# Kernel optimization log

Hardware: AMD Instinct MI355X
Metric: run time of the kernel (lower is better)

Reference implementation:

```python
import jax, jax.numpy as jnp
import numpy as np

B, H, L, N = 16, 256, 4096, 64  # N = d_state//2 retained complex-conjugate modes (S4D)
EPS = 1e-5


def setup_inputs() -> dict:
    key = jax.random.key(0)
    ks = jax.random.split(key, 6)
    x = jax.random.normal(ks[0], (B, H, L), dtype=jnp.float32)
    # dt log-uniform in [1e-3, 1e-1] per channel (standard S4 init)
    log_dt = (jax.random.uniform(ks[1], (H,), dtype=jnp.float32)
              * (np.log(0.1) - np.log(0.001)) + np.log(0.001))
    # S4D-Lin init: A_n = -1/2 + i*pi*n
    A_re = -0.5 * jnp.ones((H, N), dtype=jnp.float32)
    A_im = jnp.pi * jnp.broadcast_to(jnp.arange(N, dtype=jnp.float32), (H, N))
    # bidirectional -> 2 channel groups of C
    C_re = jax.random.normal(ks[2], (2, H, N), dtype=jnp.float32)
    C_im = jax.random.normal(ks[3], (2, H, N), dtype=jnp.float32)
    D = jax.random.normal(ks[4], (H,), dtype=jnp.float32)
    ln_w = jnp.ones((H,), dtype=jnp.float32)
    ln_b = jnp.zeros((H,), dtype=jnp.float32)
    W_out = jax.random.normal(ks[5], (H, H), dtype=jnp.float32) / np.sqrt(H)
    b_out = jnp.zeros((H,), dtype=jnp.float32)
    return {"x": x, "log_dt": log_dt, "A_re": A_re, "A_im": A_im,
            "C_re": C_re, "C_im": C_im, "D": D,
            "ln_w": ln_w, "ln_b": ln_b, "W_out": W_out, "b_out": b_out}


def _s4_forward(x, log_dt, A_re, A_im, C_re, C_im, D, ln_w, ln_b, W_out, b_out):
    # LayerNorm over channel dim (x.transpose -> LN(d_model) -> transpose back)
    mu = jnp.mean(x, axis=1, keepdims=True)
    var = jnp.mean((x - mu) ** 2, axis=1, keepdims=True)
    z = (x - mu) * jax.lax.rsqrt(var + EPS) * ln_w[None, :, None] + ln_b[None, :, None]

    # --- S4D kernel via Vandermonde (ZOH-style discretization) ---
    A = A_re + 1j * A_im                         # (H, N)
    C = C_re + 1j * C_im                         # (2, H, N)
    dt = jnp.exp(log_dt)[:, None]                # (H, 1)
    dtA = dt * A                                 # (H, N)
    C_t = C * (jnp.exp(dtA) - 1.0) / A           # (2, H, N)
    t = jnp.arange(L, dtype=jnp.float32)
    V = jnp.exp(dtA[:, :, None] * t)             # (H, N, L) Vandermonde
    K = 2.0 * jnp.real(jnp.einsum('dhn,hnl->dhl', C_t, V))  # (2, H, L)

    # bidirectional: forward kernel padded right, backward kernel flipped, padded left
    k = jnp.pad(K[0], ((0, 0), (0, L))) + jnp.pad(K[1][:, ::-1], ((0, 0), (L, 0)))

    # FFT convolution over length 2L
    Uf = jnp.fft.rfft(z, n=2 * L)                # (B, H, L+1)
    Kf = jnp.fft.rfft(k, n=2 * L)                # (H, L+1)
    y = jnp.fft.irfft(Uf * Kf[None], n=2 * L)[..., :L]

    y = y + D[None, :, None] * z                 # skip D*u
    y = jax.nn.gelu(y)                           # S4 default activation
    # transposed position-wise output linear (postact=None -> plain Linear)
    y = jnp.einsum('oh,bhl->bol', W_out, y) + b_out[None, :, None]
    return x + y                                  # residual


def reference(x, log_dt, A_re, A_im, C_re, C_im, D, ln_w, ln_b, W_out, b_out):
    return _s4_forward(x, log_dt, A_re, A_im, C_re, C_im, D, ln_w, ln_b, W_out, b_out)
```

## Files before the change

### kernel.cpp

```cpp
#include <hip/hip_runtime.h>
#include <math.h>

#define B_ 16
#define H_ 256
#define L_ 4096
#define N_ 64
#define HN (H_*N_)
#define HL (H_*L_)
#define BHL (B_*H_*L_)

#define WVT_OFS 0
#define TM_OFS  8192
#define E2T_OFS 12288
#define MATS_PER 20480

typedef short bf16x8 __attribute__((ext_vector_type(8)));
typedef float f32x4  __attribute__((ext_vector_type(4)));

__device__ __forceinline__ unsigned int pk2(float a, float b) {
    return ((__float_as_uint(a) + 0x8000u) >> 16) |
           ((__float_as_uint(b) + 0x8000u) & 0xffff0000u);
}
__device__ __forceinline__ unsigned short bfr(float a) {
    return (unsigned short)((__float_as_uint(a) + 0x8000u) >> 16);
}
__device__ __forceinline__ float ubf(unsigned short u) {
    return __uint_as_float(((unsigned int)u) << 16);
}

__global__ void __launch_bounds__(64) mats_kernel(const float* __restrict__ log_dt,
                                                  const float* __restrict__ A_re,
                                                  const float* __restrict__ A_im,
                                                  const float* __restrict__ C_re,
                                                  const float* __restrict__ C_im,
                                                  unsigned short* __restrict__ mats,
                                                  float2* __restrict__ Wc) {
    int hd = blockIdx.x;
    int h = hd >> 1, d = hd & 1;
    int m = threadIdx.x;
    __shared__ float2 pws[65 * 64];
    __shared__ float2 c2s[64];
    __shared__ float  Karr[64];

    int i = h * 64 + m;
    float dt = expf(log_dt[h]);
    float Are = A_re[i], Aim = A_im[i];
    float dr = dt * Are, di = dt * Aim;
    float er = expf(dr);
    float wr = er * cosf(di), wi = er * sinf(di);
    float em1r = wr - 1.0f, em1i = wi;
    float inv = 1.0f / (Are * Are + Aim * Aim);
    float qr = (em1r * Are + em1i * Aim) * inv;
    float qi = (em1i * Are - em1r * Aim) * inv;
    float Cr = C_re[d * HN + i], Ci = C_im[d * HN + i];
    float2 c2;
    c2.x = 2.0f * (Cr * qr - Ci * qi);
    c2.y = 2.0f * (Cr * qi + Ci * qr);
    c2s[m] = c2;
    float pr = 1.0f, pi = 0.0f;
    for (int k = 0; k < 64; ++k) {
        float2 p; p.x = pr; p.y = pi;
        pws[k * 64 + ((m + k) & 63)] = p;
        float t = pr * wr - pi * wi;
        pi = pr * wi + pi * wr;
        pr = t;
    }
    {
        float2 p; p.x = pr; p.y = pi;
        pws[64 * 64 + ((m + 64) & 63)] = p;
        Wc[hd * 64 + m] = p;
    }
    __syncthreads();
    {
        float kk = 0.f;
        for (int mm = 0; mm < 64; ++mm) {
            float2 c = c2s[mm];
            float2 pw = pws[m * 64 + ((mm + m) & 63)];
            kk += c.x * pw.x - c.y * pw.y;
        }
        Karr[m] = kk;
    }
    __syncthreads();
    unsigned short* mb = mats + (size_t)hd * MATS_PER;
    for (int i2 = 0; i2 < 32; ++i2) {
        int e0 = 2 * i2, e1 = e0 + 1;
        int k0 = d ? e0 : 63 - e0;
        int k1 = d ? e1 : 63 - e1;
        float2 p0 = pws[k0 * 64 + ((m + k0) & 63)];
        float2 p1 = pws[k1 * 64 + ((m + k1) & 63)];
        *(unsigned int*)(mb + WVT_OFS + (2 * m) * 64 + e0)     = pk2(p0.x, p1.x);
        *(unsigned int*)(mb + WVT_OFS + (2 * m + 1) * 64 + e0) = pk2(p0.y, p1.y);
    }
    for (int i2 = 0; i2 < 32; ++i2) {
        int e0 = 2 * i2, e1 = e0 + 1;
        float v0, v1;
        if (d == 0) {
            v0 = (e0 <= m) ? Karr[m - e0] : 0.f;
            v1 = (e1 <= m) ? Karr[m - e1] : 0.f;
        } else {
            v0 = (e0 > m) ? Karr[e0 - m - 1] : 0.f;
            v1 = (e1 > m) ? Karr[e1 - m - 1] : 0.f;
        }
        *(unsigned int*)(mb + TM_OFS + m * 64 + e0) = pk2(v0, v1);
    }
    {
        int kp = d ? (63 - m) : (m + 1);
        for (int mm = 0; mm < 64; ++mm) {
            float2 c = c2s[mm];
            float2 pw = pws[kp * 64 + ((mm + kp) & 63)];
            float vr = c.x * pw.x - c.y * pw.y;
            float vi = -(c.x * pw.y + c.y * pw.x);
            *(unsigned int*)(mb + E2T_OFS + m * 128 + 2 * mm) = pk2(vr, vi);
        }
    }
}

__global__ void __launch_bounds__(256) wbf_kernel(const float* __restrict__ W,
                                                  unsigned short* __restrict__ Wbf) {
    int i = (blockIdx.x * 256 + threadIdx.x) * 4;
    float4 v = *(const float4*)(W + i);
    uint2 u;
    u.x = pk2(v.x, v.y);
    u.y = pk2(v.z, v.w);
    *(uint2*)(Wbf + i) = u;
}

__global__ void __launch_bounds__(256) ln_kernel(const float* __restrict__ x,
                                                 const float* __restrict__ lnw,
                                                 const float* __restrict__ lnb,
                                                 unsigned short* __restrict__ zb) {
    int b  = blockIdx.y;
    int l0 = blockIdx.x * 256;
    int t  = threadIdx.x;
    int hq = t >> 6, lo = t & 63;
    int l  = l0 + lo * 4;
    __shared__ float4 r1[4][64];
    __shared__ float4 r2[4][64];
    __shared__ float4 muS[64];
    __shared__ float4 rsS[64];
    const float* xb = x + (size_t)b * HL;
    float4 s1 = {0.f,0.f,0.f,0.f}, s2 = {0.f,0.f,0.f,0.f};
    #pragma unroll 4
    for (int hh = 0; hh < 64; ++hh) {
        int h = hq * 64 + hh;
        float4 v = *(const float4*)(xb + (size_t)h * L_ + l);
        s1.x += v.x; s1.y += v.y; s1.z += v.z; s1.w += v.w;
        s2.x += v.x*v.x; s2.y += v.y*v.y; s2.z += v.z*v.z; s2.w += v.w*v.w;
    }
    r1[hq][lo] = s1; r2[hq][lo] = s2;
    __syncthreads();
    if (t < 64) {
        float4 S1 = r1[0][t], S2 = r2[0][t];
        #pragma unroll
        for (int q = 1; q < 4; ++q) {
            float4 a = r1[q][t], c = r2[q][t];
            S1.x += a.x; S1.y += a.y; S1.z += a.z; S1.w += a.w;
            S2.x += c.x; S2.y += c.y; S2.z += c.z; S2.w += c.w;
        }
        const float invH = 1.0f / 256.0f;
        float4 mu, rs;
        mu.x = S1.x*invH; mu.y = S1.y*invH; mu.z = S1.z*invH; mu.w = S1.w*invH;
        rs.x = rsqrtf(S2.x*invH - mu.x*mu.x + 1e-5f);
        rs.y = rsqrtf(S2.y*invH - mu.y*mu.y + 1e-5f);
        rs.z = rsqrtf(S2.z*invH - mu.z*mu.z + 1e-5f);
        rs.w = rsqrtf(S2.w*invH - mu.w*mu.w + 1e-5f);
        muS[t] = mu; rsS[t] = rs;
    }
    __syncthreads();
    float4 mu = muS[lo], rs = rsS[lo];
    #pragma unroll 4
    for (int hh = 0; hh < 64; ++hh) {
        int h = hq * 64 + hh;
        float w = lnw[h], bb = lnb[h];
        float4 v = *(const float4*)(xb + (size_t)h * L_ + l);
        float4 zz;
        zz.x = (v.x - mu.x) * rs.x * w + bb;
        zz.y = (v.y - mu.y) * rs.y * w + bb;
        zz.z = (v.z - mu.z) * rs.z * w + bb;
        zz.w = (v.w - mu.w) * rs.w * w + bb;
        uint2 u;
        u.x = pk2(zz.x, zz.y);
        u.y = pk2(zz.z, zz.w);
        *(uint2*)(zb + (size_t)b * HL + (size_t)h * L_ + l) = u;
    }
}

#define MFMA16(a,b,c) __builtin_amdgcn_mfma_f32_16x16x32_bf16((a),(b),(c),0,0,0)
#define SU_BASE 8192
#define GST_BASE 32768

__global__ void __launch_bounds__(256, 3) ssm_kernel(const unsigned short* __restrict__ zb,
                                                     const unsigned short* __restrict__ mats,
                                                     const float2* __restrict__ Wc,
                                                     const float* __restrict__ D,
                                                     unsigned short* __restrict__ gb) {
    int bh = blockIdx.x;
    int h  = bh & (H_ - 1);
    int t  = threadIdx.x;
    int w  = t >> 6, l = t & 63;
    int d  = w >> 1, p = w & 1;

    __shared__ __align__(16) char smem[40960];

    const unsigned short* mb = mats + (size_t)(h * 2 + d) * MATS_PER;

    {
        const char* zrow = (const char*)(zb + (size_t)bh * L_);
        #pragma unroll
        for (int k = 0; k < 2; ++k) {
            int row = w * 16 + k * 8 + (l >> 3);
            int chunk = (l & 7) ^ (row & 7);
            const char* src = zrow + row * 128 + chunk * 16;
            __builtin_amdgcn_global_load_lds(
                (const __attribute__((address_space(1))) unsigned int*)src,
                (__attribute__((address_space(3))) unsigned int*)(smem + w * 2048 + k * 1024),
                16, 0, 0);
        }
    }
    __syncthreads();

    bf16x8 za[4][2];
    int arow = l & 15;
    int koff = (l >> 4) * 8;
    #pragma unroll
    for (int cb = 0; cb < 4; ++cb) {
        int row = cb * 16 + arow;
        unsigned int sw = (row & 7) << 4;
        #pragma unroll
        for (int kb = 0; kb < 2; ++kb) {
            unsigned int byte = (unsigned)(row * 128 + (kb * 32 + koff) * 2) ^ sw;
            za[cb][kb] = *(bf16x8*)(smem + byte);
        }
    }

    char* sUd = smem + SU_BASE + d * 16384;
    #pragma unroll
    for (int mcb = 0; mcb < 4; ++mcb) {
        int mcblk = p * 4 + mcb;
        const unsigned short* wv = mb + WVT_OFS + (mcblk * 16 + arow) * 64 + koff;
        bf16x8 b0 = *(const bf16x8*)(wv);
        bf16x8 b1 = *(const bf16x8*)(wv + 32);
        #pragma unroll
        for (int cb = 0; cb < 4; ++cb) {
            f32x4 acc = {0.f, 0.f, 0.f, 0.f};
            acc = MFMA16(za[cb][0], b0, acc);
            acc = MFMA16(za[cb][1], b1, acc);
            int mc = mcblk * 16 + arow;
            #pragma unroll
            for (int rr = 0; rr < 4; ++rr) {
                int c = cb * 16 + (l >> 4) * 4 + rr;
                unsigned int byte = ((unsigned)(c * 256 + mc * 2)) ^ ((c & 7) << 4);
                *(unsigned short*)(sUd + byte) = bfr(acc[rr]);
            }
        }
    }
    __syncthreads();

    if (p == 0) {
        float2 w64 = Wc[(h * 2 + d) * 64 + l];
        float sr = 0.f, si = 0.f;
        if (d == 0) {
            for (int c = 0; c < 64; ++c) {
                unsigned int byte = ((unsigned)(c * 256 + l * 4)) ^ ((c & 7) << 4);
                unsigned int uu = *(unsigned int*)(sUd + byte);
                float ur = __uint_as_float(uu << 16);
                float ui = __uint_as_float(uu & 0xffff0000u);
                *(unsigned int*)(sUd + byte) = pk2(sr, si);
                float nsr = fmaf(w64.x, sr, fmaf(-w64.y, si, ur));
                float nsi = fmaf(w64.x, si, fmaf(w64.y, sr, ui));
                sr = nsr; si = nsi;
            }
        } else {
            for (int c = 63; c >= 0; --c) {
                unsigned int byte = ((unsigned)(c * 256 + l * 4)) ^ ((c & 7) << 4);
                unsigned int uu = *(unsigned int*)(sUd + byte);
                float ur = __uint_as_float(uu << 16);
                float ui = __uint_as_float(uu & 0xffff0000u);
                *(unsigned int*)(sUd + byte) = pk2(sr, si);
                float nsr = fmaf(w64.x, sr, fmaf(-w64.y, si, ur));
                float nsi = fmaf(w64.x, si, fmaf(w64.y, sr, ui));
                sr = nsr; si = nsi;
            }
        }
    }
    __syncthreads();

    f32x4 yacc[2][4];
    #pragma unroll
    for (int jb = 0; jb < 2; ++jb) {
        int jblk = p * 2 + jb;
        const unsigned short* tm = mb + TM_OFS + (jblk * 16 + arow) * 64 + koff;
        bf16x8 tb0 = *(const bf16x8*)(tm);
        bf16x8 tb1 = *(const bf16x8*)(tm + 32);
        const unsigned short* et = mb + E2T_OFS + (jblk * 16 + arow) * 128 + koff;
        bf16x8 eb0 = *(const bf16x8*)(et);
        bf16x8 eb1 = *(const bf16x8*)(et + 32);
        bf16x8 eb2 = *(const bf16x8*)(et + 64);
        bf16x8 eb3 = *(const bf16x8*)(et + 96);
        #pragma unroll
        for (int cb = 0; cb < 4; ++cb) {
            f32x4 acc = {0.f, 0.f, 0.f, 0.f};
            acc = MFMA16(za[cb][0], tb0, acc);
            acc = MFMA16(za[cb][1], tb1, acc);
            int row = cb * 16 + arow;
            unsigned int sw = (row & 7) << 4;
            bf16x8 sa0 = *(bf16x8*)(sUd + (((unsigned)(row * 256 + (0 * 32 + koff) * 2)) ^ sw));
            bf16x8 sa1 = *(bf16x8*)(sUd + (((unsigned)(row * 256 + (1 * 32 + koff) * 2)) ^ sw));
            bf16x8 sa2 = *(bf16x8*)(sUd + (((unsigned)(row * 256 + (2 * 32 + koff) * 2)) ^ sw));
            bf16x8 sa3 = *(bf16x8*)(sUd + (((unsigned)(row * 256 + (3 * 32 + koff) * 2)) ^ sw));
            acc = MFMA16(sa0, eb0, acc);
            acc = MFMA16(sa1, eb1, acc);
            acc = MFMA16(sa2, eb2, acc);
            acc = MFMA16(sa3, eb3, acc);
            yacc[jb][cb] = acc;
        }
    }
    __syncthreads();

    float* Yb = (float*)(smem + SU_BASE);
    if (d == 1) {
        #pragma unroll
        for (int jb = 0; jb < 2; ++jb) {
            int j = (p * 2 + jb) * 16 + arow;
            #pragma unroll
            for (int cb = 0; cb < 4; ++cb) {
                #pragma unroll
                for (int rr = 0; rr < 4; ++rr) {
                    int c = cb * 16 + (l >> 4) * 4 + rr;
                    Yb[c * 66 + j] = yacc[jb][cb][rr];
                }
            }
        }
    }
    __syncthreads();
    if (d == 0) {
        float dv = D[h];
        #pragma unroll
        for (int jb = 0; jb < 2; ++jb) {
            int j = (p * 2 + jb) * 16 + arow;
            #pragma unroll
            for (int cb = 0; cb < 4; ++cb) {
                #pragma unroll
                for (int rr = 0; rr < 4; ++rr) {
                    int c = cb * 16 + (l >> 4) * 4 + rr;
                    unsigned int zbyte = ((unsigned)(c * 128 + j * 2)) ^ ((c & 7) << 4);
                    float zv = ubf(*(unsigned short*)(smem + zbyte));
                    float y = yacc[jb][cb][rr] + Yb[c * 66 + j] + dv * zv;
                    float inner = 0.7978845608028654f * (y + 0.044715f * y * y * y);
                    float gv = 0.5f * y * (1.0f + tanhf(inner));
                    *(unsigned short*)(smem + GST_BASE + zbyte) = bfr(gv);
                }
            }
        }
    }
    __syncthreads();
    {
        int c2 = t >> 2, s2 = t & 3;
        unsigned int rsw = (c2 & 7) << 4;
        char* go = (char*)(gb + (size_t)bh * L_);
        uint4 a0 = *(const uint4*)(smem + GST_BASE + (((unsigned)(c2 * 128 + s2 * 32)) ^ rsw));
        uint4 a1 = *(const uint4*)(smem + GST_BASE + (((unsigned)(c2 * 128 + s2 * 32 + 16)) ^ rsw));
        *(uint4*)(go + c2 * 128 + s2 * 32)      = a0;
        *(uint4*)(go + c2 * 128 + s2 * 32 + 16) = a1;
    }
}

__global__ void __launch_bounds__(256, 4) gt_kernel(const unsigned short* __restrict__ gb,
                                                    unsigned short* __restrict__ gT) {
    int b  = blockIdx.y;
    int l0 = blockIdx.x * 64;
    int t  = threadIdx.x;
    __shared__ __align__(16) char lT[64 * 512];
    const unsigned short* gp = gb + ((size_t)b * H_ + t) * L_ + l0;
    uint4 v[8];
    #pragma unroll
    for (int j8 = 0; j8 < 8; ++j8) v[j8] = *(const uint4*)(gp + j8 * 8);
    #pragma unroll
    for (int j8 = 0; j8 < 8; ++j8) {
        #pragma unroll
        for (int e = 0; e < 8; ++e) {
            int l = j8 * 8 + e;
            unsigned short val = ((const unsigned short*)&v[j8])[e];
            *(unsigned short*)(lT + (((unsigned)(l * 512 + t * 2)) ^ ((l & 7) << 4))) = val;
        }
    }
    __syncthreads();
    int l = t >> 2, seg = t & 3;
    unsigned short* dst = gT + ((size_t)b * L_ + l0 + l) * 256 + seg * 64;
    unsigned int sw = (l & 7) << 4;
    #pragma unroll
    for (int j = 0; j < 8; ++j) {
        uint4 u = *(const uint4*)(lT + (((unsigned)(l * 512 + seg * 128 + j * 16)) ^ sw));
        *(uint4*)(dst + j * 8) = u;
    }
}

__global__ void __launch_bounds__(256, 3) outproj_kernel(
        const unsigned short* __restrict__ gT,
        const unsigned short* __restrict__ Wbf,
        const float* __restrict__ x,
        const float* __restrict__ bias,
        float* __restrict__ out) {
    int b  = blockIdx.z;
    int o0 = blockIdx.y * 128;
    int l0 = blockIdx.x * 128;
    int t  = threadIdx.x;
    int w  = t >> 6, lane = t & 63;
    int wr = w >> 1, wc = w & 1;
    int l15 = lane & 15, q = lane >> 4;

    __shared__ __align__(16) char lds[34816];
    unsigned short* At = (unsigned short*)lds;
    unsigned short* Bt = (unsigned short*)(lds + 16384);

    f32x4 acc[4][4];
    #pragma unroll
    for (int i = 0; i < 4; ++i)
        #pragma unroll
        for (int j = 0; j < 4; ++j) acc[i][j] = (f32x4){0.f, 0.f, 0.f, 0.f};

    const unsigned short* gTb = gT + ((size_t)b * L_ + l0) * 256;
    const unsigned short* Wb0 = Wbf + (size_t)o0 * 256;
    unsigned int swz = (unsigned)(l15 & 7) << 4;

    for (int kt = 0; kt < 4; ++kt) {
        int k0 = kt * 64;
        #pragma unroll
        for (int s = 0; s < 4; ++s) {
            int id = (w * 4 + s) * 64 + lane;
            int row = id >> 3, ch = id & 7;
            int chl = ch ^ (row & 7);
            uint4 va = *(const uint4*)(gTb + (size_t)row * 256 + k0 + chl * 8);
            uint4 vb = *(const uint4*)(Wb0 + (size_t)row * 256 + k0 + chl * 8);
            *(uint4*)(At + id * 8) = va;
            *(uint4*)(Bt + id * 8) = vb;
        }
        __syncthreads();
        #pragma unroll
        for (int kk = 0; kk < 2; ++kk) {
            bf16x8 af[4], bfr_[4];
            #pragma unroll
            for (int rb = 0; rb < 4; ++rb) {
                int li = wr * 64 + rb * 16 + l15;
                af[rb] = *(const bf16x8*)((char*)At + li * 128 + (((kk * 64 + q * 16)) ^ swz));
                int oi = wc * 64 + rb * 16 + l15;
                bfr_[rb] = *(const bf16x8*)((char*)Bt + oi * 128 + (((kk * 64 + q * 16)) ^ swz));
            }
            #pragma unroll
            for (int rb = 0; rb < 4; ++rb)
                #pragma unroll
                for (int cb = 0; cb < 4; ++cb)
                    acc[rb][cb] = MFMA16(af[rb], bfr_[cb], acc[rb][cb]);
        }
        __syncthreads();
    }

    float* Eb = (float*)lds;
    for (int pp = 0; pp < 2; ++pp) {
        if (wc == pp) {
            #pragma unroll
            for (int cb = 0; cb < 4; ++cb) {
                int o_loc = cb * 16 + l15;
                unsigned int esw = (unsigned)(o_loc & 7) << 4;
                #pragma unroll
                for (int rb = 0; rb < 4; ++rb) {
                    int colbase = wr * 64 + rb * 16 + q * 4;
                    #pragma unroll
                    for (int r = 0; r < 4; ++r) {
                        int col = colbase + r;
                        *(float*)((char*)Eb + o_loc * 528 + (((unsigned)(col * 4)) ^ esw)) =
                            acc[rb][cb][r];
                    }
                }
            }
        }
        __syncthreads();
        int o_loc = t >> 2, lseg = t & 3;
        int o = o0 + pp * 64 + o_loc;
        float bo = bias[o];
        unsigned int esw = (unsigned)(o_loc & 7) << 4;
        size_t off = ((size_t)b * H_ + o) * L_ + l0 + lseg * 32;
        const float* xr = x + off;
        float* orow = out + off;
        #pragma unroll
        for (int j = 0; j < 8; ++j) {
            float4 e = *(const float4*)((char*)Eb + o_loc * 528 +
                                        (((unsigned)(lseg * 128 + j * 16)) ^ esw));
            float4 xv = *(const float4*)(xr + j * 4);
            float4 ov;
            ov.x = xv.x + bo + e.x;
            ov.y = xv.y + bo + e.y;
            ov.z = xv.z + bo + e.z;
            ov.w = xv.w + bo + e.w;
            *(float4*)(orow + j * 4) = ov;
        }
        __syncthreads();
    }
}

extern "C" void kernel_launch(void* const* d_in, const int* in_sizes, int n_in,
                              void* d_out, int out_size, void* d_ws, size_t ws_size,
                              hipStream_t stream) {
    const float* x      = (const float*)d_in[0];
    const float* log_dt = (const float*)d_in[1];
    const float* A_re   = (const float*)d_in[2];
    const float* A_im   = (const float*)d_in[3];
    const float* C_re   = (const float*)d_in[4];
    const float* C_im   = (const float*)d_in[5];
    const float* D      = (const float*)d_in[6];
    const float* lnw    = (const float*)d_in[7];
    const float* lnb    = (const float*)d_in[8];
    const float* W      = (const float*)d_in[9];
    const float* bout   = (const float*)d_in[10];
    float* out = (float*)d_out;

    unsigned short* zb   = (unsigned short*)d_ws;
    unsigned short* gb   = zb + (size_t)BHL;
    unsigned short* gT   = gb + (size_t)BHL;
    unsigned short* mats = gT + (size_t)BHL;
    float2* Wc = (float2*)(mats + 512 * (size_t)MATS_PER);
    unsigned short* Wbf = (unsigned short*)(Wc + 512 * 64);

    mats_kernel<<<512, 64, 0, stream>>>(log_dt, A_re, A_im, C_re, C_im, mats, Wc);
    wbf_kernel<<<64, 256, 0, stream>>>(W, Wbf);
    ln_kernel<<<dim3(L_ / 256, B_), 256, 0, stream>>>(x, lnw, lnb, zb);
    ssm_kernel<<<B_ * H_, 256, 0, stream>>>(zb, mats, Wc, D, gb);
    gt_kernel<<<dim3(L_ / 64, B_), 256, 0, stream>>>(gb, gT);
    outproj_kernel<<<dim3(L_ / 128, H_ / 128, B_), 256, 0, stream>>>(gT, Wbf, x, bout, out);
}
```

Baseline: 208.7 us.

## Split SSM directions into separate blocks and fuse combine+GELU into transpose

Each SSM block now handles one direction (forward or backward) with 128 threads, so there are twice as many blocks, each using less shared memory, and the in-block cross-direction reduction through LDS is gone. Each block writes its partial output as bf16 to a separate buffer. The transpose kernel then reads both partials plus z, applies the D skip and a tanh-form GELU written with exp and a reciprocal, and writes the transposed result. This adds an extra BHL bf16 buffer of global traffic and rounds the partial outputs to bf16 before they are summed.

```diff
diff --git a/kernel.cpp b/kernel.cpp
--- a/kernel.cpp
+++ b/kernel.cpp
@@ -187,33 +187,34 @@
 
 #define MFMA16(a,b,c) __builtin_amdgcn_mfma_f32_16x16x32_bf16((a),(b),(c),0,0,0)
 #define SU_BASE 8192
-#define GST_BASE 32768
-
-__global__ void __launch_bounds__(256, 3) ssm_kernel(const unsigned short* __restrict__ zb,
+
+__global__ void __launch_bounds__(128, 3) ssm_kernel(const unsigned short* __restrict__ zb,
                                                      const unsigned short* __restrict__ mats,
                                                      const float2* __restrict__ Wc,
-                                                     const float* __restrict__ D,
-                                                     unsigned short* __restrict__ gb) {
-    int bh = blockIdx.x;
+                                                     unsigned short* __restrict__ yf,
+                                                     unsigned short* __restrict__ yb) {
+    int bhd = blockIdx.x;
+    int d  = bhd & 1;
+    int bh = bhd >> 1;
     int h  = bh & (H_ - 1);
     int t  = threadIdx.x;
     int w  = t >> 6, l = t & 63;
-    int d  = w >> 1, p = w & 1;
-
-    __shared__ __align__(16) char smem[40960];
+    int p  = w;
+
+    __shared__ __align__(16) char smem[24576];
 
     const unsigned short* mb = mats + (size_t)(h * 2 + d) * MATS_PER;
 
     {
         const char* zrow = (const char*)(zb + (size_t)bh * L_);
         #pragma unroll
-        for (int k = 0; k < 2; ++k) {
-            int row = w * 16 + k * 8 + (l >> 3);
+        for (int k = 0; k < 4; ++k) {
+            int row = w * 32 + k * 8 + (l >> 3);
             int chunk = (l & 7) ^ (row & 7);
             const char* src = zrow + row * 128 + chunk * 16;
             __builtin_amdgcn_global_load_lds(
                 (const __attribute__((address_space(1))) unsigned int*)src,
-                (__attribute__((address_space(3))) unsigned int*)(smem + w * 2048 + k * 1024),
+                (__attribute__((address_space(3))) unsigned int*)(smem + w * 4096 + k * 1024),
                 16, 0, 0);
         }
     }
@@ -233,7 +234,7 @@
         }
     }
 
-    char* sUd = smem + SU_BASE + d * 16384;
+    char* sUd = smem + SU_BASE;
     #pragma unroll
     for (int mcb = 0; mcb < 4; ++mcb) {
         int mcblk = p * 4 + mcb;
@@ -317,71 +318,63 @@
     }
     __syncthreads();
 
-    float* Yb = (float*)(smem + SU_BASE);
-    if (d == 1) {
-        #pragma unroll
-        for (int jb = 0; jb < 2; ++jb) {
-            int j = (p * 2 + jb) * 16 + arow;
+    #pragma unroll
+    for (int jb = 0; jb < 2; ++jb) {
+        int j = (p * 2 + jb) * 16 + arow;
+        #pragma unroll
+        for (int cb = 0; cb < 4; ++cb) {
             #pragma unroll
-            for (int cb = 0; cb < 4; ++cb) {
-                #pragma unroll
-                for (int rr = 0; rr < 4; ++rr) {
-                    int c = cb * 16 + (l >> 4) * 4 + rr;
-                    Yb[c * 66 + j] = yacc[jb][cb][rr];
-                }
+            for (int rr = 0; rr < 4; ++rr) {
+                int c = cb * 16 + (l >> 4) * 4 + rr;
+                unsigned int byte = ((unsigned)(c * 128 + j * 2)) ^ ((c & 7) << 4);
+                *(unsigned short*)(smem + byte) = bfr(yacc[jb][cb][rr]);
             }
         }
     }
     __syncthreads();
-    if (d == 0) {
-        float dv = D[h];
-        #pragma unroll
-        for (int jb = 0; jb < 2; ++jb) {
-            int j = (p * 2 + jb) * 16 + arow;
-            #pragma unroll
-            for (int cb = 0; cb < 4; ++cb) {
-                #pragma unroll
-                for (int rr = 0; rr < 4; ++rr) {
-                    int c = cb * 16 + (l >> 4) * 4 + rr;
-                    unsigned int zbyte = ((unsigned)(c * 128 + j * 2)) ^ ((c & 7) << 4);
-                    float zv = ubf(*(unsigned short*)(smem + zbyte));
-                    float y = yacc[jb][cb][rr] + Yb[c * 66 + j] + dv * zv;
-                    float inner = 0.7978845608028654f * (y + 0.044715f * y * y * y);
-                    float gv = 0.5f * y * (1.0f + tanhf(inner));
-                    *(unsigned short*)(smem + GST_BASE + zbyte) = bfr(gv);
-                }
-            }
-        }
-    }
-    __syncthreads();
     {
-        int c2 = t >> 2, s2 = t & 3;
-        unsigned int rsw = (c2 & 7) << 4;
-        char* go = (char*)(gb + (size_t)bh * L_);
-        uint4 a0 = *(const uint4*)(smem + GST_BASE + (((unsigned)(c2 * 128 + s2 * 32)) ^ rsw));
-        uint4 a1 = *(const uint4*)(smem + GST_BASE + (((unsigned)(c2 * 128 + s2 * 32 + 16)) ^ rsw));
-        *(uint4*)(go + c2 * 128 + s2 * 32)      = a0;
-        *(uint4*)(go + c2 * 128 + s2 * 32 + 16) = a1;
-    }
-}
-
-__global__ void __launch_bounds__(256, 4) gt_kernel(const unsigned short* __restrict__ gb,
+        int row = t >> 1, halfq = t & 1;
+        unsigned int rsw = (row & 7) << 4;
+        char* go = (char*)((d ? yb : yf) + (size_t)bh * L_);
+        #pragma unroll
+        for (int j = 0; j < 4; ++j) {
+            unsigned int off = (unsigned)(row * 128 + halfq * 64 + j * 16);
+            uint4 a = *(const uint4*)(smem + (off ^ rsw));
+            *(uint4*)(go + off) = a;
+        }
+    }
+}
+
+__global__ void __launch_bounds__(256, 4) gt_kernel(const unsigned short* __restrict__ yf,
+                                                    const unsigned short* __restrict__ yb,
+                                                    const unsigned short* __restrict__ zbuf,
+                                                    const float* __restrict__ D,
                                                     unsigned short* __restrict__ gT) {
     int b  = blockIdx.y;
     int l0 = blockIdx.x * 64;
     int t  = threadIdx.x;
     __shared__ __align__(16) char lT[64 * 512];
-    const unsigned short* gp = gb + ((size_t)b * H_ + t) * L_ + l0;
-    uint4 v[8];
-    #pragma unroll
-    for (int j8 = 0; j8 < 8; ++j8) v[j8] = *(const uint4*)(gp + j8 * 8);
+    size_t base = ((size_t)b * H_ + t) * L_ + l0;
+    const uint4* yfp = (const uint4*)(yf + base);
+    const uint4* ybp = (const uint4*)(yb + base);
+    const uint4* zp  = (const uint4*)(zbuf + base);
+    float dh = D[t];
     #pragma unroll
     for (int j8 = 0; j8 < 8; ++j8) {
+        uint4 a = yfp[j8];
+        uint4 c = ybp[j8];
+        uint4 z4 = zp[j8];
         #pragma unroll
         for (int e = 0; e < 8; ++e) {
             int l = j8 * 8 + e;
-            unsigned short val = ((const unsigned short*)&v[j8])[e];
-            *(unsigned short*)(lT + (((unsigned)(l * 512 + t * 2)) ^ ((l & 7) << 4))) = val;
+            float vf = ubf(((const unsigned short*)&a)[e]);
+            float vb = ubf(((const unsigned short*)&c)[e]);
+            float vz = ubf(((const unsigned short*)&z4)[e]);
+            float y = vf + vb + dh * vz;
+            float inner = 0.7978845608028654f * (y + 0.044715f * y * y * y);
+            float en = __expf(-2.0f * inner);
+            float g = y * __builtin_amdgcn_rcpf(1.0f + en);
+            *(unsigned short*)(lT + (((unsigned)(l * 512 + t * 2)) ^ ((l & 7) << 4))) = bfr(g);
         }
     }
     __syncthreads();
@@ -515,8 +508,9 @@
     float* out = (float*)d_out;
 
     unsigned short* zb   = (unsigned short*)d_ws;
-    unsigned short* gb   = zb + (size_t)BHL;
-    unsigned short* gT   = gb + (size_t)BHL;
+    unsigned short* yf   = zb + (size_t)BHL;
+    unsigned short* yb   = yf + (size_t)BHL;
+    unsigned short* gT   = yb + (size_t)BHL;
     unsigned short* mats = gT + (size_t)BHL;
     float2* Wc = (float2*)(mats + 512 * (size_t)MATS_PER);
     unsigned short* Wbf = (unsigned short*)(Wc + 512 * 64);
@@ -524,7 +518,7 @@
     mats_kernel<<<512, 64, 0, stream>>>(log_dt, A_re, A_im, C_re, C_im, mats, Wc);
     wbf_kernel<<<64, 256, 0, stream>>>(W, Wbf);
     ln_kernel<<<dim3(L_ / 256, B_), 256, 0, stream>>>(x, lnw, lnb, zb);
-    ssm_kernel<<<B_ * H_, 256, 0, stream>>>(zb, mats, Wc, D, gb);
-    gt_kernel<<<dim3(L_ / 64, B_), 256, 0, stream>>>(gb, gT);
+    ssm_kernel<<<B_ * H_ * 2, 128, 0, stream>>>(zb, mats, Wc, yf, yb);
+    gt_kernel<<<dim3(L_ / 64, B_), 256, 0, stream>>>(yf, yb, zb, D, gT);
     outproj_kernel<<<dim3(L_ / 128, H_ / 128, B_), 256, 0, stream>>>(gT, Wbf, x, bout, out);
 }
```

New measurement: 278.4 us. 1.33x slower.
